# Kernel optimization log

Measured on AMD Instinct MI355X. Metric: run time of the kernel, lower is better.

## Reference

```python
import jax, jax.numpy as jnp
import numpy as np

USER_COUNT = 200000
ITEM_COUNT = 100000
N_NODES = USER_COUNT + ITEM_COUNT
EMB = 64
NNZ = 9600000
N_LAYERS = 3
BATCH = 4096
VAL_SCALE = 0.03125  # ~1/avg_degree, mimics symmetric degree normalization of norm_adj


def setup_inputs() -> dict:
    key = jax.random.key(0)
    k1, k2, k3, k4, k5, k6, k7 = jax.random.split(key, 7)
    user_emb = jax.random.normal(k1, (USER_COUNT, EMB), dtype=jnp.float32)
    item_emb = jax.random.normal(k2, (ITEM_COUNT, EMB), dtype=jnp.float32)
    adj_row = jnp.sort(jax.random.randint(k3, (NNZ,), 0, N_NODES, dtype=jnp.int64))
    adj_col = jax.random.randint(k4, (NNZ,), 0, N_NODES, dtype=jnp.int64)
    adj_val = jax.random.uniform(k5, (NNZ,), dtype=jnp.float32) * VAL_SCALE
    users = jax.random.randint(k6, (BATCH,), 0, USER_COUNT, dtype=jnp.int64)
    items = jax.random.randint(k7, (BATCH,), 0, ITEM_COUNT, dtype=jnp.int64)
    return {"user_emb": user_emb, "item_emb": item_emb, "adj_row": adj_row,
            "adj_col": adj_col, "adj_val": adj_val, "users": users, "items": items}


def _spmm(row, col, val, x):
    # sparse [N,N] @ dense [N,E] via gather + segment-sum
    return jax.ops.segment_sum(val[:, None] * x[col], row, num_segments=N_NODES)


def reference(user_emb, item_emb, adj_row, adj_col, adj_val, users, items):
    ego = jnp.concatenate([user_emb, item_emb], axis=0)  # [N, E]
    acc = ego  # running sum across layer outputs (== stack+mean fused)
    h = ego
    for _ in range(N_LAYERS):
        h = _spmm(adj_row, adj_col, adj_val, h)
        acc = acc + h
    all_emb = acc / jnp.float32(N_LAYERS + 1)
    u_all = all_emb[:USER_COUNT]
    i_all = all_emb[USER_COUNT:]
    return (u_all[users], i_all[items])
```

## Files before the change

### kernel.cpp

```cpp
#include <hip/hip_runtime.h>

#define USER_COUNT 200000
#define ITEM_COUNT 100000
#define N_NODES    300000
#define EMB        64
#define BATCH      4096

typedef unsigned int   u32;
typedef unsigned short u16;
typedef u16   ushort8v __attribute__((ext_vector_type(8)));
typedef float float8v  __attribute__((ext_vector_type(8)));

static __device__ __forceinline__ float bf2f(u16 h) {
    return __uint_as_float(((u32)h) << 16);
}
static __device__ __forceinline__ u16 f2bf(float f) {
    u32 u = __float_as_uint(f);
    u32 r = (u + 0x7FFFu + ((u >> 16) & 1u)) >> 16;
    return (u16)r;
}

__global__ void build_row_ptr(const int* __restrict__ row,
                              int* __restrict__ ptr, int nnz) {
    int i = blockIdx.x * blockDim.x + threadIdx.x;
    if (i >= nnz) return;
    int r  = row[i];
    int rp = (i == 0) ? -1 : row[i - 1];
    for (int rr = rp + 1; rr <= r; ++rr) ptr[rr] = i;
    if (i == nnz - 1) {
        for (int rr = r + 1; rr <= N_NODES; ++rr) ptr[rr] = nnz;
    }
}

__global__ void convert_bf16(const float* __restrict__ ue,
                             const float* __restrict__ ie,
                             u16* __restrict__ out16) {
    size_t t = (size_t)blockIdx.x * blockDim.x + threadIdx.x;
    const size_t total = (size_t)N_NODES * EMB / 4;
    if (t >= total) return;
    size_t base = t * 4;
    const size_t ub = (size_t)USER_COUNT * EMB;
    const float* src = (base < ub) ? (ue + base) : (ie + (base - ub));
    float4 v = *(const float4*)src;
    ushort4 o;
    o.x = f2bf(v.x); o.y = f2bf(v.y); o.z = f2bf(v.z); o.w = f2bf(v.w);
    *(ushort4*)(out16 + base) = o;
}

__global__ void mark_needed(const int* __restrict__ users,
                            const int* __restrict__ items,
                            const int* __restrict__ col,
                            const int* __restrict__ ptr,
                            u32* __restrict__ flag) {
    int slot = (int)((blockIdx.x * blockDim.x + threadIdx.x) >> 6);
    if (slot >= 2 * BATCH) return;
    int lane = threadIdx.x & 63;
    int row = (slot < BATCH) ? users[slot] : (items[slot - BATCH] + USER_COUNT);
    if (lane == 0) flag[row] = 1;
    int p0 = ptr[row];
    int p1 = ptr[row + 1];
    for (int j = p0 + lane; j < p1; j += 64) flag[col[j]] = 1;
}

#define EDGE_FMA8P(BASE, ACC)                                         \
    {                                                                 \
        int  jj = (BASE) + e;                                         \
        int  jc = (jj < p1) ? jj : (p1 - 1);                          \
        int   c = __builtin_nontemporal_load(col + jc);               \
        float v = __builtin_nontemporal_load(val + jc);               \
        v = (jj < p1) ? v : 0.0f;                                     \
        ushort8v h8 = *(const ushort8v*)(x + (size_t)c * EMB + d);    \
        _Pragma("unroll")                                             \
        for (int q = 0; q < 8; ++q) ACC[q] += v * bf2f(h8[q]);        \
    }

#define SLOT_REDUCE(ACC)                                              \
    _Pragma("unroll")                                                 \
    for (int q = 0; q < 8; ++q) {                                     \
        ACC[q] += __shfl_xor(ACC[q], 8, 64);                          \
        ACC[q] += __shfl_xor(ACC[q], 16, 64);                        \
        ACC[q] += __shfl_xor(ACC[q], 32, 64);                        \
    }

template <bool USE_FLAG>
__global__ __launch_bounds__(256) void spmm_bf16(
        const u16* __restrict__ x, const int* __restrict__ col,
        const float* __restrict__ val, const int* __restrict__ ptr,
        const u32* __restrict__ flag, u16* __restrict__ y) {
    int wave = (int)((blockIdx.x * blockDim.x + threadIdx.x) >> 6);
    int lane = threadIdx.x & 63;
    if (wave >= N_NODES) return;
    if (USE_FLAG && flag[wave] == 0) return;
    int e = lane >> 3;
    int d = (lane & 7) << 3;

    int p0 = ptr[wave];
    int p1 = ptr[wave + 1];

    float8v a0 = {0,0,0,0,0,0,0,0};
    float8v a1 = {0,0,0,0,0,0,0,0};

    for (int base = p0; base < p1; base += 16) {
        EDGE_FMA8P(base,     a0);
        EDGE_FMA8P(base + 8, a1);
    }

    #pragma unroll
    for (int q = 0; q < 8; ++q) a0[q] += a1[q];

    SLOT_REDUCE(a0);

    if (e == 0) {
        ushort8v o;
        #pragma unroll
        for (int q = 0; q < 8; ++q) o[q] = f2bf(a0[q]);
        *(ushort8v*)(y + (size_t)wave * EMB + d) = o;
    }
}

__global__ __launch_bounds__(256) void spmm_bf16_sel(
        const u16* __restrict__ x, const int* __restrict__ col,
        const float* __restrict__ val, const int* __restrict__ ptr,
        const int* __restrict__ users, const int* __restrict__ items,
        float* __restrict__ out) {
    int slot = (int)((blockIdx.x * blockDim.x + threadIdx.x) >> 6);
    if (slot >= 2 * BATCH) return;
    int lane = threadIdx.x & 63;
    int e = lane >> 3;
    int d = (lane & 7) << 3;

    int row = (slot < BATCH) ? users[slot] : (items[slot - BATCH] + USER_COUNT);
    int p0 = ptr[row];
    int p1 = ptr[row + 1];

    float8v a0 = {0,0,0,0,0,0,0,0};
    float8v a1 = {0,0,0,0,0,0,0,0};

    for (int base = p0; base < p1; base += 16) {
        EDGE_FMA8P(base,     a0);
        EDGE_FMA8P(base + 8, a1);
    }

    #pragma unroll
    for (int q = 0; q < 8; ++q) a0[q] += a1[q];

    SLOT_REDUCE(a0);

    if (e == 0) {
        float* o = out + (size_t)slot * EMB + d;
        float4 c0 = *(float4*)o;
        float4 c1 = *(float4*)(o + 4);
        c0.x += 0.25f * a0[0]; c0.y += 0.25f * a0[1];
        c0.z += 0.25f * a0[2]; c0.w += 0.25f * a0[3];
        c1.x += 0.25f * a0[4]; c1.y += 0.25f * a0[5];
        c1.z += 0.25f * a0[6]; c1.w += 0.25f * a0[7];
        *(float4*)o       = c0;
        *(float4*)(o + 4) = c1;
    }
}

__global__ void gather_f32(const float* __restrict__ xu,
                           const float* __restrict__ xi,
                           const int* __restrict__ users,
                           const int* __restrict__ items,
                           float* __restrict__ out) {
    int tid = blockIdx.x * blockDim.x + threadIdx.x;
    if (tid >= 2 * BATCH * (EMB / 4)) return;
    int b = tid >> 4;
    int e = (tid & 15) << 2;
    const float* src;
    if (b < BATCH) src = xu + (size_t)users[b] * EMB + e;
    else           src = xi + (size_t)items[b - BATCH] * EMB + e;
    float4 s = *(const float4*)src;
    float4 v = {0.25f * s.x, 0.25f * s.y, 0.25f * s.z, 0.25f * s.w};
    *(float4*)(out + (size_t)b * EMB + e) = v;
}

__global__ void gather_bf16_add(const u16* __restrict__ h,
                                const int* __restrict__ users,
                                const int* __restrict__ items,
                                float* __restrict__ out) {
    int tid = blockIdx.x * blockDim.x + threadIdx.x;
    if (tid >= 2 * BATCH * (EMB / 4)) return;
    int b = tid >> 4;
    int e = (tid & 15) << 2;
    int row = (b < BATCH) ? users[b] : (items[b - BATCH] + USER_COUNT);
    ushort4 s = *(const ushort4*)(h + (size_t)row * EMB + e);
    float4* o = (float4*)(out + (size_t)b * EMB + e);
    float4 cur = *o;
    cur.x += 0.25f * bf2f(s.x);
    cur.y += 0.25f * bf2f(s.y);
    cur.z += 0.25f * bf2f(s.z);
    cur.w += 0.25f * bf2f(s.w);
    *o = cur;
}

extern "C" void kernel_launch(void* const* d_in, const int* in_sizes, int n_in,
                              void* d_out, int out_size, void* d_ws, size_t ws_size,
                              hipStream_t stream) {
    const float* user_emb = (const float*)d_in[0];
    const float* item_emb = (const float*)d_in[1];
    const int*   adj_row  = (const int*)d_in[2];
    const int*   adj_col  = (const int*)d_in[3];
    const float* adj_val  = (const float*)d_in[4];
    const int*   users    = (const int*)d_in[5];
    const int*   items    = (const int*)d_in[6];
    float*       out      = (float*)d_out;
    const int    nnz      = in_sizes[2];

    char* ws = (char*)d_ws;
    const size_t hbytes = (size_t)N_NODES * EMB * sizeof(u16);
    u16* ego16 = (u16*)(ws);
    u16* h1    = (u16*)(ws + hbytes);
    u16* h2    = (u16*)(ws + 2 * hbytes);
    int* ptr   = (int*)(ws + 3 * hbytes);
    u32* flag  = (u32*)(ws + 3 * hbytes + (size_t)(N_NODES + 64) * sizeof(int));

    hipMemsetAsync(flag, 0, (size_t)N_NODES * sizeof(u32), stream);

    build_row_ptr<<<(nnz + 255) / 256, 256, 0, stream>>>(adj_row, ptr, nnz);

    {
        const size_t total = (size_t)N_NODES * EMB / 4;
        convert_bf16<<<(unsigned)((total + 255) / 256), 256, 0, stream>>>(
            user_emb, item_emb, ego16);
    }

    mark_needed<<<(2 * BATCH + 3) / 4, 256, 0, stream>>>(
        users, items, adj_col, ptr, flag);

    const int gthreads = 2 * BATCH * (EMB / 4);
    gather_f32<<<(gthreads + 255) / 256, 256, 0, stream>>>(
        user_emb, item_emb, users, items, out);

    const int spmm_blocks = (N_NODES + 3) / 4;

    spmm_bf16<false><<<spmm_blocks, 256, 0, stream>>>(
        ego16, adj_col, adj_val, ptr, nullptr, h1);
    gather_bf16_add<<<(gthreads + 255) / 256, 256, 0, stream>>>(h1, users, items, out);

    spmm_bf16<true><<<spmm_blocks, 256, 0, stream>>>(
        h1, adj_col, adj_val, ptr, flag, h2);
    gather_bf16_add<<<(gthreads + 255) / 256, 256, 0, stream>>>(h2, users, items, out);

    spmm_bf16_sel<<<(2 * BATCH + 3) / 4, 256, 0, stream>>>(
        h2, adj_col, adj_val, ptr, users, items, out);
}
```

Baseline: 385.3 us.

## Interleave column index and value into packed edge array, split loop tail

Adds a pre-pass that packs each edge's column index and value into one 8-byte int2 entry, so the SpMM kernels fetch both with a single load instead of two separate streams. The main edge loop now runs full 16-edge chunks without bounds predication and handles only the final partial chunk with clamped loads. Output stores become nontemporal. The packing pass costs an extra read of col/val and a write of the packed array each call. It is used only when the workspace is large enough, otherwise the old path runs.

```diff
diff --git a/kernel.cpp b/kernel.cpp
--- a/kernel.cpp
+++ b/kernel.cpp
@@ -10,6 +10,7 @@
 typedef unsigned short u16;
 typedef u16   ushort8v __attribute__((ext_vector_type(8)));
 typedef float float8v  __attribute__((ext_vector_type(8)));
+typedef int   int2v    __attribute__((ext_vector_type(2)));
 
 static __device__ __forceinline__ float bf2f(u16 h) {
     return __uint_as_float(((u32)h) << 16);
@@ -30,6 +31,17 @@
     if (i == nnz - 1) {
         for (int rr = r + 1; rr <= N_NODES; ++rr) ptr[rr] = nnz;
     }
+}
+
+__global__ void build_cv(const int* __restrict__ col,
+                         const float* __restrict__ val,
+                         int2v* __restrict__ cv, int nnz) {
+    int i = blockIdx.x * blockDim.x + threadIdx.x;
+    if (i >= nnz) return;
+    int2v t;
+    t.x = col[i];
+    t.y = __float_as_int(val[i]);
+    __builtin_nontemporal_store(t, cv + i);
 }
 
 __global__ void convert_bf16(const float* __restrict__ ue,
@@ -62,31 +74,61 @@
     for (int j = p0 + lane; j < p1; j += 64) flag[col[j]] = 1;
 }
 
-#define EDGE_FMA8P(BASE, ACC)                                         \
-    {                                                                 \
-        int  jj = (BASE) + e;                                         \
-        int  jc = (jj < p1) ? jj : (p1 - 1);                          \
-        int   c = __builtin_nontemporal_load(col + jc);               \
-        float v = __builtin_nontemporal_load(val + jc);               \
-        v = (jj < p1) ? v : 0.0f;                                     \
-        ushort8v h8 = *(const ushort8v*)(x + (size_t)c * EMB + d);    \
-        _Pragma("unroll")                                             \
-        for (int q = 0; q < 8; ++q) ACC[q] += v * bf2f(h8[q]);        \
-    }
+template <bool USE_CV>
+static __device__ __forceinline__ void load_edge(
+        const int2v* __restrict__ cv, const int* __restrict__ col,
+        const float* __restrict__ val, int j, int& c, float& v) {
+    if (USE_CV) {
+        int2v t = __builtin_nontemporal_load(cv + j);
+        c = t.x; v = __int_as_float(t.y);
+    } else {
+        c = __builtin_nontemporal_load(col + j);
+        v = __builtin_nontemporal_load(val + j);
+    }
+}
+
+template <bool USE_CV>
+static __device__ __forceinline__ void edge_clean(
+        const u16* __restrict__ x, const int2v* cv, const int* col,
+        const float* val, int j, int d, float8v& acc) {
+    int c; float v;
+    load_edge<USE_CV>(cv, col, val, j, c, v);
+    ushort8v h8 = *(const ushort8v*)(x + (size_t)c * EMB + d);
+    float8v xf;
+    #pragma unroll
+    for (int q = 0; q < 8; ++q) xf[q] = bf2f(h8[q]);
+    acc += v * xf;
+}
+
+template <bool USE_CV>
+static __device__ __forceinline__ void edge_pred(
+        const u16* __restrict__ x, const int2v* cv, const int* col,
+        const float* val, int jj, int p1, int p1m1, int d, float8v& acc) {
+    int jc = (jj < p1) ? jj : p1m1;
+    int c; float v;
+    load_edge<USE_CV>(cv, col, val, jc, c, v);
+    v = (jj < p1) ? v : 0.0f;
+    ushort8v h8 = *(const ushort8v*)(x + (size_t)c * EMB + d);
+    float8v xf;
+    #pragma unroll
+    for (int q = 0; q < 8; ++q) xf[q] = bf2f(h8[q]);
+    acc += v * xf;
+}
 
 #define SLOT_REDUCE(ACC)                                              \
     _Pragma("unroll")                                                 \
     for (int q = 0; q < 8; ++q) {                                     \
         ACC[q] += __shfl_xor(ACC[q], 8, 64);                          \
-        ACC[q] += __shfl_xor(ACC[q], 16, 64);                        \
-        ACC[q] += __shfl_xor(ACC[q], 32, 64);                        \
-    }
-
-template <bool USE_FLAG>
+        ACC[q] += __shfl_xor(ACC[q], 16, 64);                         \
+        ACC[q] += __shfl_xor(ACC[q], 32, 64);                         \
+    }
+
+template <bool USE_FLAG, bool USE_CV>
 __global__ __launch_bounds__(256) void spmm_bf16(
-        const u16* __restrict__ x, const int* __restrict__ col,
-        const float* __restrict__ val, const int* __restrict__ ptr,
-        const u32* __restrict__ flag, u16* __restrict__ y) {
+        const u16* __restrict__ x, const int2v* __restrict__ cv,
+        const int* __restrict__ col, const float* __restrict__ val,
+        const int* __restrict__ ptr, const u32* __restrict__ flag,
+        u16* __restrict__ y) {
     int wave = (int)((blockIdx.x * blockDim.x + threadIdx.x) >> 6);
     int lane = threadIdx.x & 63;
     if (wave >= N_NODES) return;
@@ -100,9 +142,15 @@
     float8v a0 = {0,0,0,0,0,0,0,0};
     float8v a1 = {0,0,0,0,0,0,0,0};
 
-    for (int base = p0; base < p1; base += 16) {
-        EDGE_FMA8P(base,     a0);
-        EDGE_FMA8P(base + 8, a1);
+    int base = p0;
+    for (; base + 16 <= p1; base += 16) {
+        edge_clean<USE_CV>(x, cv, col, val, base + e,     d, a0);
+        edge_clean<USE_CV>(x, cv, col, val, base + 8 + e, d, a1);
+    }
+    if (base < p1) {
+        int p1m1 = p1 - 1;
+        edge_pred<USE_CV>(x, cv, col, val, base + e,     p1, p1m1, d, a0);
+        edge_pred<USE_CV>(x, cv, col, val, base + 8 + e, p1, p1m1, d, a1);
     }
 
     #pragma unroll
@@ -114,15 +162,16 @@
         ushort8v o;
         #pragma unroll
         for (int q = 0; q < 8; ++q) o[q] = f2bf(a0[q]);
-        *(ushort8v*)(y + (size_t)wave * EMB + d) = o;
-    }
-}
-
+        __builtin_nontemporal_store(o, (ushort8v*)(y + (size_t)wave * EMB + d));
+    }
+}
+
+template <bool USE_CV>
 __global__ __launch_bounds__(256) void spmm_bf16_sel(
-        const u16* __restrict__ x, const int* __restrict__ col,
-        const float* __restrict__ val, const int* __restrict__ ptr,
-        const int* __restrict__ users, const int* __restrict__ items,
-        float* __restrict__ out) {
+        const u16* __restrict__ x, const int2v* __restrict__ cv,
+        const int* __restrict__ col, const float* __restrict__ val,
+        const int* __restrict__ ptr, const int* __restrict__ users,
+        const int* __restrict__ items, float* __restrict__ out) {
     int slot = (int)((blockIdx.x * blockDim.x + threadIdx.x) >> 6);
     if (slot >= 2 * BATCH) return;
     int lane = threadIdx.x & 63;
@@ -136,9 +185,15 @@
     float8v a0 = {0,0,0,0,0,0,0,0};
     float8v a1 = {0,0,0,0,0,0,0,0};
 
-    for (int base = p0; base < p1; base += 16) {
-        EDGE_FMA8P(base,     a0);
-        EDGE_FMA8P(base + 8, a1);
+    int base = p0;
+    for (; base + 16 <= p1; base += 16) {
+        edge_clean<USE_CV>(x, cv, col, val, base + e,     d, a0);
+        edge_clean<USE_CV>(x, cv, col, val, base + 8 + e, d, a1);
+    }
+    if (base < p1) {
+        int p1m1 = p1 - 1;
+        edge_pred<USE_CV>(x, cv, col, val, base + e,     p1, p1m1, d, a0);
+        edge_pred<USE_CV>(x, cv, col, val, base + 8 + e, p1, p1m1, d, a1);
     }
 
     #pragma unroll
@@ -215,10 +270,16 @@
     u16* h2    = (u16*)(ws + 2 * hbytes);
     int* ptr   = (int*)(ws + 3 * hbytes);
     u32* flag  = (u32*)(ws + 3 * hbytes + (size_t)(N_NODES + 64) * sizeof(int));
+    size_t fixed = 3 * hbytes + 2 * (size_t)(N_NODES + 64) * sizeof(int);
+    bool use_cv = (fixed + (size_t)nnz * 8 + 256) <= ws_size;
+    int2v* cv = (int2v*)(ws + ((fixed + 255) & ~(size_t)255));
 
     hipMemsetAsync(flag, 0, (size_t)N_NODES * sizeof(u32), stream);
 
     build_row_ptr<<<(nnz + 255) / 256, 256, 0, stream>>>(adj_row, ptr, nnz);
+
+    if (use_cv)
+        build_cv<<<(nnz + 255) / 256, 256, 0, stream>>>(adj_col, adj_val, cv, nnz);
 
     {
         const size_t total = (size_t)N_NODES * EMB / 4;
@@ -234,15 +295,25 @@
         user_emb, item_emb, users, items, out);
 
     const int spmm_blocks = (N_NODES + 3) / 4;
-
-    spmm_bf16<false><<<spmm_blocks, 256, 0, stream>>>(
-        ego16, adj_col, adj_val, ptr, nullptr, h1);
-    gather_bf16_add<<<(gthreads + 255) / 256, 256, 0, stream>>>(h1, users, items, out);
-
-    spmm_bf16<true><<<spmm_blocks, 256, 0, stream>>>(
-        h1, adj_col, adj_val, ptr, flag, h2);
-    gather_bf16_add<<<(gthreads + 255) / 256, 256, 0, stream>>>(h2, users, items, out);
-
-    spmm_bf16_sel<<<(2 * BATCH + 3) / 4, 256, 0, stream>>>(
-        h2, adj_col, adj_val, ptr, users, items, out);
-}
+    const int sel_blocks  = (2 * BATCH + 3) / 4;
+
+    if (use_cv) {
+        spmm_bf16<false, true><<<spmm_blocks, 256, 0, stream>>>(
+            ego16, cv, adj_col, adj_val, ptr, nullptr, h1);
+        gather_bf16_add<<<(gthreads + 255) / 256, 256, 0, stream>>>(h1, users, items, out);
+        spmm_bf16<true, true><<<spmm_blocks, 256, 0, stream>>>(
+            h1, cv, adj_col, adj_val, ptr, flag, h2);
+        gather_bf16_add<<<(gthreads + 255) / 256, 256, 0, stream>>>(h2, users, items, out);
+        spmm_bf16_sel<true><<<sel_blocks, 256, 0, stream>>>(
+            h2, cv, adj_col, adj_val, ptr, users, items, out);
+    } else {
+        spmm_bf16<false, false><<<spmm_blocks, 256, 0, stream>>>(
+            ego16, nullptr, adj_col, adj_val, ptr, nullptr, h1);
+        gather_bf16_add<<<(gthreads + 255) / 256, 256, 0, stream>>>(h1, users, items, out);
+        spmm_bf16<true, false><<<spmm_blocks, 256, 0, stream>>>(
+            h1, nullptr, adj_col, adj_val, ptr, flag, h2);
+        gather_bf16_add<<<(gthreads + 255) / 256, 256, 0, stream>>>(h2, users, items, out);
+        spmm_bf16_sel<false><<<sel_blocks, 256, 0, stream>>>(
+            h2, nullptr, adj_col, adj_val, ptr, users, items, out);
+    }
+}
```

New measurement: 418.0 us. +8.5%, slower.
